# Kernel optimization log

Measured on AMD Instinct MI355X. Metric: run time of the kernel, lower is better.

## Reference

```python
import jax, jax.numpy as jnp
import numpy as np

N_S, N_T, E = 50000, 50000, 600000
D_IN, D_H, D_OUT = 256, 128, 64


def setup_inputs() -> dict:
    key = jax.random.key(0)
    k1, k2, k3, k4, k5, k6 = jax.random.split(key, 6)
    edge_src = jax.random.randint(k1, (E,), 0, N_S, dtype=jnp.int32)
    edge_dst = jax.random.randint(k2, (E,), 0, N_T, dtype=jnp.int32)
    edge_index = jnp.stack([edge_src, edge_dst], axis=0)  # [2, E]
    x_s = jax.random.normal(k3, (N_S, D_IN), dtype=jnp.float32)
    x_t = jax.random.normal(k4, (N_T, D_IN), dtype=jnp.float32)
    W0 = jax.random.normal(k5, (D_IN, D_H), dtype=jnp.float32) * (1.0 / np.sqrt(D_IN))
    W1 = jax.random.normal(k6, (D_H, D_OUT), dtype=jnp.float32) * (1.0 / np.sqrt(D_H))
    return {"edge_index": edge_index, "x_s": x_s, "x_t": x_t, "W0": W0, "W1": W1}


def gcn_conv(x, src, dst, W):
    """PyG GCNConv, bias=False: D^{-1/2}(A+I)D^{-1/2} (x @ W)."""
    N = x.shape[0]
    h = x @ W  # [N, out]
    loops = jnp.arange(N, dtype=src.dtype)
    s = jnp.concatenate([src, loops])  # add self-loops
    d = jnp.concatenate([dst, loops])
    deg = jax.ops.segment_sum(jnp.ones_like(d, dtype=h.dtype), d, num_segments=N)
    dinv = jnp.where(deg > 0, jax.lax.rsqrt(deg), 0.0)
    norm = dinv[s] * dinv[d]  # [E+N]
    return jax.ops.segment_sum(h[s] * norm[:, None], d, num_segments=N)


def reference(edge_index, x_s, x_t, W0, W1):
    n_s = x_s.shape[0]
    src = edge_index[0]
    dst = edge_index[1] + n_s  # targets live in the x_t block
    acts = [jax.nn.relu, lambda v: v]
    Ws = [W0, W1]
    for W, act in zip(Ws, acts):
        x = jnp.concatenate([x_s, x_t], axis=0)
        x = act(gcn_conv(x, src, dst, W))
        x_s, x_t = x[:n_s], x[n_s:]
    return (x_s, x_t)
```

## Files before the change

### kernel.cpp

```cpp
#include <hip/hip_runtime.h>
#include <cstdint>
#include <cstddef>

typedef unsigned short u16;
typedef unsigned int   u32;
typedef __attribute__((ext_vector_type(8))) short bf16x8;
typedef __attribute__((ext_vector_type(4))) float f32x4;

#define D_IN  256
#define D_H   128
#define D_OUT 64

__device__ __forceinline__ float bf2f(u16 u){
  union { u32 i; float f; } v; v.i = ((u32)u) << 16; return v.f;
}
__device__ __forceinline__ u16 f2bf(float f){
  union { float f; u32 i; } v; v.f = f;
  u32 r = (v.i + 0x7fffu + ((v.i >> 16) & 1u)) >> 16;
  return (u16)r;
}

__global__ void k_wprep(const float* __restrict__ W0, const float* __restrict__ W1,
                        u16* __restrict__ W0t, u16* __restrict__ W1t){
  int i = blockIdx.x * 256 + threadIdx.x;
  if (i < 128 * 256){
    int n = i >> 8, k = i & 255;
    W0t[i] = f2bf(W0[(size_t)k * 128 + n]);
  } else if (i < 128 * 256 + 64 * 128){
    int j = i - 128 * 256;
    int n = j >> 7, k = j & 127;
    W1t[j] = f2bf(W1[(size_t)k * 64 + n]);
  }
}

__global__ __launch_bounds__(256) void k_off(const int* __restrict__ deg, int N,
                                             int* __restrict__ off, int* __restrict__ cursor,
                                             float* __restrict__ dinv){
  __shared__ int s[256];
  __shared__ int sbase[256];
  const int tid = threadIdx.x;
  const int bid = blockIdx.x;
  const int i   = bid * 256 + tid;
  int acc = 0;
  const int lim = bid * 256;
  for (int j = tid; j < lim; j += 256) acc += deg[j];
  sbase[tid] = acc;
  int v = (i < N) ? deg[i] : 0;
  s[tid] = v;
  __syncthreads();
  for (int o = 128; o > 0; o >>= 1){
    if (tid < o) sbase[tid] += sbase[tid + o];
    __syncthreads();
  }
  for (int o = 1; o < 256; o <<= 1){
    int tv = (tid >= o) ? s[tid - o] : 0;
    __syncthreads();
    s[tid] += tv;
    __syncthreads();
  }
  if (i < N){
    int excl = s[tid] - v + sbase[0];
    off[i] = excl;
    cursor[i] = excl;
    dinv[i] = rsqrtf((float)v + 1.0f);
  }
}

__global__ void k_fill(const int* __restrict__ src, const int* __restrict__ dst,
                       int E, int* __restrict__ cursor, int* __restrict__ csr){
  int e = blockIdx.x * 256 + threadIdx.x;
  if (e < E){
    int d = dst[e];
    int p = atomicAdd(&cursor[d], 1);
    csr[p] = src[e];
  }
}

__global__ __launch_bounds__(512) void k_g1(
    const float* __restrict__ Xs, const float* __restrict__ Xt,
    const u16* __restrict__ W0t, int M, int n_s,
    const int* __restrict__ dst, int E, int* __restrict__ deg, int nbDeg,
    u16* __restrict__ out)
{
  __shared__ u16 Bs[128 * 256];
  const int t = threadIdx.x;

  if ((int)blockIdx.x < nbDeg){
    const int stride = nbDeg * 512;
    for (int e = blockIdx.x * 512 + t; e < E; e += stride)
      atomicAdd(&deg[dst[e]], 1);
    return;
  }

  const int wave = t >> 6, lane = t & 63;
  const int lm   = lane & 15, quad = lane >> 4;
  const int gw   = ((int)blockIdx.x - nbDeg) * 8 + wave;
  const int row  = gw * 16 + lm;

  int cr = (row < M) ? row : 0;
  const float* pa = ((cr < n_s) ? (Xs + (size_t)cr * D_IN)
                                : (Xt + (size_t)(cr - n_s) * D_IN)) + quad * 8;

  f32x4 A[16];
  asm volatile("global_load_dwordx4 %0, %1, off offset:0"   : "=v"(A[ 0]) : "v"(pa));
  asm volatile("global_load_dwordx4 %0, %1, off offset:16"  : "=v"(A[ 1]) : "v"(pa));
  asm volatile("global_load_dwordx4 %0, %1, off offset:128" : "=v"(A[ 2]) : "v"(pa));
  asm volatile("global_load_dwordx4 %0, %1, off offset:144" : "=v"(A[ 3]) : "v"(pa));
  asm volatile("global_load_dwordx4 %0, %1, off offset:256" : "=v"(A[ 4]) : "v"(pa));
  asm volatile("global_load_dwordx4 %0, %1, off offset:272" : "=v"(A[ 5]) : "v"(pa));
  asm volatile("global_load_dwordx4 %0, %1, off offset:384" : "=v"(A[ 6]) : "v"(pa));
  asm volatile("global_load_dwordx4 %0, %1, off offset:400" : "=v"(A[ 7]) : "v"(pa));
  asm volatile("global_load_dwordx4 %0, %1, off offset:512" : "=v"(A[ 8]) : "v"(pa));
  asm volatile("global_load_dwordx4 %0, %1, off offset:528" : "=v"(A[ 9]) : "v"(pa));
  asm volatile("global_load_dwordx4 %0, %1, off offset:640" : "=v"(A[10]) : "v"(pa));
  asm volatile("global_load_dwordx4 %0, %1, off offset:656" : "=v"(A[11]) : "v"(pa));
  asm volatile("global_load_dwordx4 %0, %1, off offset:768" : "=v"(A[12]) : "v"(pa));
  asm volatile("global_load_dwordx4 %0, %1, off offset:784" : "=v"(A[13]) : "v"(pa));
  asm volatile("global_load_dwordx4 %0, %1, off offset:896" : "=v"(A[14]) : "v"(pa));
  asm volatile("global_load_dwordx4 %0, %1, off offset:912" : "=v"(A[15]) : "v"(pa));

  {
    const int n = t >> 2;
    const int c = t & 3;
    const u16* wsrc = W0t + (size_t)n * 256 + c * 64;
    char* brow = (char*)Bs + n * 512;
    const int sw = (n & 15) << 4;
    #pragma unroll
    for (int j = 0; j < 8; j++){
      int off = (c * 128 + j * 16) ^ sw;
      *(int4*)(brow + off) = *(const int4*)(wsrc + j * 8);
    }
  }

  f32x4 acc[8];
  const f32x4 z = {0.f, 0.f, 0.f, 0.f};
  #pragma unroll
  for (int nf = 0; nf < 8; nf++) acc[nf] = z;

  __syncthreads();
  asm volatile("s_waitcnt vmcnt(0)" ::: "memory");
  __builtin_amdgcn_sched_barrier(0);

  const char* bb = (const char*)Bs + lm * 512;
  const int lmx = lm << 4;

  #pragma unroll
  for (int kk = 0; kk < 8; kk++){
    bf16x8 af;
    {
      f32x4 lo = A[2 * kk], hi = A[2 * kk + 1];
      u16 tmp[8];
      tmp[0] = f2bf(lo[0]); tmp[1] = f2bf(lo[1]);
      tmp[2] = f2bf(lo[2]); tmp[3] = f2bf(lo[3]);
      tmp[4] = f2bf(hi[0]); tmp[5] = f2bf(hi[1]);
      tmp[6] = f2bf(hi[2]); tmp[7] = f2bf(hi[3]);
      af = *(const bf16x8*)tmp;
    }
    const int koff = (kk * 64 + quad * 16) ^ lmx;
    #pragma unroll
    for (int nf = 0; nf < 8; nf++){
      bf16x8 bf = *(const bf16x8*)(bb + nf * 8192 + koff);
      acc[nf] = __builtin_amdgcn_mfma_f32_16x16x32_bf16(af, bf, acc[nf], 0, 0, 0);
    }
  }

  __syncthreads();
  u16* wreg = Bs + wave * 2048;
  #pragma unroll
  for (int nf = 0; nf < 8; nf++){
    #pragma unroll
    for (int rr = 0; rr < 4; rr++){
      int rl = quad * 4 + rr;
      int c  = nf * 16 + lm;
      wreg[rl * 128 + (c ^ (quad << 5))] = f2bf(acc[nf][rr]);
    }
  }
  {
    const int g = lane >> 4, l = lane & 15;
    const int wrow0 = gw * 16;
    #pragma unroll
    for (int i = 0; i < 4; i++){
      int rl = i * 4 + g;
      int m  = wrow0 + rl;
      bf16x8 v = *(const bf16x8*)&wreg[rl * 128 + ((l ^ (i << 2)) << 3)];
      if (m < M) *(bf16x8*)(out + (size_t)m * D_H + l * 8) = v;
    }
  }
}

__device__ __forceinline__ void aggf_body(
    const int* __restrict__ off, const int* __restrict__ deg,
    const int* __restrict__ csr, const float* __restrict__ dinv,
    u16* __restrict__ h1, int n_s, int n_t, int w, int lane)
{
  if (w >= n_t) return;
  const int g = lane >> 4;
  const int c = lane & 15;
  int start = off[w];
  int n     = deg[w];

  float r[8], p[8];
  #pragma unroll
  for (int q = 0; q < 8; q++){ r[q] = 0.f; p[q] = 0.f; }

  int i = 0;
  for (; i + 8 <= n; i += 8){
    int sa = csr[start + i + g];
    int sb = csr[start + i + 4 + g];
    int4 da = *(const int4*)(h1 + (size_t)sa * D_H + c * 8);
    int4 db = *(const int4*)(h1 + (size_t)sb * D_H + c * 8);
    const u16* ha = (const u16*)&da;
    const u16* hb = (const u16*)&db;
    #pragma unroll
    for (int q = 0; q < 8; q++){
      float va = bf2f(ha[q]), vb = bf2f(hb[q]);
      r[q] += va + vb;
      p[q] += fmaxf(va, 0.f) + fmaxf(vb, 0.f);
    }
  }
  for (; i < n; i += 4){
    if (i + g < n){
      int sa = csr[start + i + g];
      int4 da = *(const int4*)(h1 + (size_t)sa * D_H + c * 8);
      const u16* ha = (const u16*)&da;
      #pragma unroll
      for (int q = 0; q < 8; q++){
        float va = bf2f(ha[q]);
        r[q] += va;
        p[q] += fmaxf(va, 0.f);
      }
    }
  }

  #pragma unroll
  for (int q = 0; q < 8; q++){
    r[q] += __shfl_xor(r[q], 16, 64);
    r[q] += __shfl_xor(r[q], 32, 64);
    p[q] += __shfl_xor(p[q], 16, 64);
    p[q] += __shfl_xor(p[q], 32, 64);
  }

  if (g == 0){
    float di  = dinv[w];
    float di2 = di * di;
    u16* selfp = h1 + (size_t)(n_s + w) * D_H + c * 8;
    int4 hs = *(const int4*)selfp;
    const u16* hh = (const u16*)&hs;
    u16 ob[8];
    #pragma unroll
    for (int q = 0; q < 8; q++){
      float zq = fmaxf(di * r[q] + di2 * bf2f(hh[q]), 0.f);
      float uq = di * p[q] + di2 * zq;
      ob[q] = f2bf(uq);
    }
    *(int4*)selfp = *(int4*)ob;
  }
}

__device__ __forceinline__ bf16x8 relu_bf(int4 v, bool relu){
  const u16* s = (const u16*)&v;
  u16 tmp[8];
  #pragma unroll
  for (int q = 0; q < 8; q++){
    u16 x = s[q];
    tmp[q] = (relu && (x & 0x8000u)) ? (u16)0 : x;
  }
  return *(const bf16x8*)tmp;
}

__device__ __forceinline__ void gemm2_body(
    const u16* __restrict__ h1, const u16* __restrict__ W1t,
    int gb, int base, int rowLim, int n_s, float* __restrict__ out,
    u16* Bs, float* Cb)
{
  const int t    = threadIdx.x;
  const int wave = t >> 6, lane = t & 63;
  const int lm   = lane & 15, quad = lane >> 4;
  const int gw   = gb * 8 + wave;
  const int row  = base + gw * 16 + lm;

  int cr = (row < rowLim) ? row : base;
  const bool relu = (cr < n_s);
  const u16* pa = h1 + (size_t)cr * D_H + quad * 8;

  int4 a[4];
  a[0] = *(const int4*)(pa);
  a[1] = *(const int4*)(pa + 32);

  {
    const int n = t >> 3;
    const int c = t & 7;
    const u16* wsrc = W1t + (size_t)n * 128 + c * 16;
    char* brow = (char*)Bs + n * 256;
    const int sw = (n & 15) << 4;
    #pragma unroll
    for (int j = 0; j < 2; j++){
      int off = (c * 32 + j * 16) ^ sw;
      *(int4*)(brow + off) = *(const int4*)(wsrc + j * 8);
    }
  }
  a[2] = *(const int4*)(pa + 64);
  a[3] = *(const int4*)(pa + 96);
  __builtin_amdgcn_sched_barrier(0);

  f32x4 acc[4];
  const f32x4 z = {0.f, 0.f, 0.f, 0.f};
  #pragma unroll
  for (int nf = 0; nf < 4; nf++) acc[nf] = z;

  __syncthreads();

  const char* bb = (const char*)Bs + lm * 256;
  const int lmx = lm << 4;

  #pragma unroll
  for (int kk = 0; kk < 4; kk++){
    bf16x8 af = relu_bf(a[kk], relu);
    const int koff = (kk * 64 + quad * 16) ^ lmx;
    #pragma unroll
    for (int nf = 0; nf < 4; nf++){
      bf16x8 bf = *(const bf16x8*)(bb + nf * 4096 + koff);
      acc[nf] = __builtin_amdgcn_mfma_f32_16x16x32_bf16(af, bf, acc[nf], 0, 0, 0);
    }
  }

  float* wreg = Cb + wave * 1024;
  #pragma unroll
  for (int nf = 0; nf < 4; nf++){
    #pragma unroll
    for (int rr = 0; rr < 4; rr++){
      int rl = quad * 4 + rr;
      int c  = nf * 16 + lm;
      wreg[rl * 64 + (c ^ (quad << 4))] = acc[nf][rr];
    }
  }
  {
    const int g = lane >> 4, l = lane & 15;
    const int wrow0 = base + gw * 16;
    #pragma unroll
    for (int i = 0; i < 4; i++){
      int rl = i * 4 + g;
      int m  = wrow0 + rl;
      float4 v = *(const float4*)&wreg[rl * 64 + ((l ^ (i << 2)) << 2)];
      if (m < rowLim) *(float4*)(out + (size_t)m * D_OUT + l * 4) = v;
    }
  }
}

__global__ __launch_bounds__(512, 4) void k_agg2s(
    const int* __restrict__ off, const int* __restrict__ deg,
    const int* __restrict__ csr, const float* __restrict__ dinv,
    u16* __restrict__ h1, int n_s, int n_t,
    const u16* __restrict__ W1t, float* __restrict__ out, int nbAgg)
{
  __shared__ u16  Bs[64 * 128];
  __shared__ float Cb[8 * 1024];
  if ((int)blockIdx.x < nbAgg){
    int w = blockIdx.x * 8 + (threadIdx.x >> 6);
    aggf_body(off, deg, csr, dinv, h1, n_s, n_t, w, threadIdx.x & 63);
  } else {
    gemm2_body(h1, W1t, (int)blockIdx.x - nbAgg, 0, n_s, n_s, out, Bs, Cb);
  }
}

__global__ __launch_bounds__(512, 4) void k_g2t(
    const u16* __restrict__ h1, const u16* __restrict__ W1t,
    int M, int n_s, float* __restrict__ out)
{
  __shared__ u16  Bs[64 * 128];
  __shared__ float Cb[8 * 1024];
  gemm2_body(h1, W1t, (int)blockIdx.x, n_s, M, n_s, out, Bs, Cb);
}

static inline size_t alup(size_t x){ return (x + 255) & ~(size_t)255; }

extern "C" void kernel_launch(void* const* d_in, const int* in_sizes, int n_in,
                              void* d_out, int out_size, void* d_ws, size_t ws_size,
                              hipStream_t stream)
{
  const int*   ei = (const int*)d_in[0];
  const float* xs = (const float*)d_in[1];
  const float* xt = (const float*)d_in[2];
  const float* W0 = (const float*)d_in[3];
  const float* W1 = (const float*)d_in[4];
  const int E   = in_sizes[0] / 2;
  const int n_s = in_sizes[1] / D_IN;
  const int n_t = in_sizes[2] / D_IN;
  const int M   = n_s + n_t;
  const int* src = ei;
  const int* dst = ei + E;

  char* p = (char*)d_ws;
  int*   deg    = (int*)p;    p += alup((size_t)n_t * 4);
  int*   off    = (int*)p;    p += alup((size_t)n_t * 4);
  int*   cursor = (int*)p;    p += alup((size_t)n_t * 4);
  float* dinv   = (float*)p;  p += alup((size_t)n_t * 4);
  int*   csr    = (int*)p;    p += alup((size_t)E * 4);
  u16*   W0t    = (u16*)p;    p += alup((size_t)D_H * D_IN * 2);
  u16*   W1t    = (u16*)p;    p += alup((size_t)D_OUT * D_H * 2);
  u16*   h1     = (u16*)p;    p += alup((size_t)M * D_H * 2);

  const int nb_t   = (n_t + 255) / 256;
  const int nbDeg  = 128;
  const int nbG1   = (M + 127) / 128;
  const int nbAgg  = (n_t + 7) / 8;
  const int nbG2s  = (n_s + 127) / 128;
  const int nbG2t  = (n_t + 127) / 128;

  hipMemsetAsync(deg, 0, (size_t)n_t * 4, stream);
  k_wprep <<<160, 256, 0, stream>>>(W0, W1, W0t, W1t);
  k_g1    <<<nbDeg + nbG1, 512, 0, stream>>>(xs, xt, W0t, M, n_s, dst, E, deg, nbDeg, h1);
  k_off   <<<nb_t, 256, 0, stream>>>(deg, n_t, off, cursor, dinv);
  k_fill  <<<(E + 255) / 256, 256, 0, stream>>>(src, dst, E, cursor, csr);
  k_agg2s <<<nbAgg + nbG2s, 512, 0, stream>>>(off, deg, csr, dinv, h1, n_s, n_t,
                                              W1t, (float*)d_out, nbAgg);
  k_g2t   <<<nbG2t, 512, 0, stream>>>(h1, W1t, M, n_s, (float*)d_out);
}
```

Baseline: 267.4 us.

## Move degree count into weight-prep kernel and overlap CSR fill with GEMM1

The degree-counting atomics now share a launch with the weight transpose/convert kernel, and the CSR fill loop is folded into the first GEMM kernel as extra leading blocks, replacing the standalone fill kernel. The aim is to overlap the scattered-atomic CSR construction with the bandwidth-heavy feature GEMM and to drop one kernel launch. In exchange, the offset/scan kernel now sits between the prep and GEMM launches, so the degree pass no longer overlaps the GEMM, and the grid-stride fill with 128 blocks may serialize behind the GEMM blocks.

```diff
diff --git a/kernel.cpp b/kernel.cpp
--- a/kernel.cpp
+++ b/kernel.cpp
@@ -20,9 +20,19 @@
   return (u16)r;
 }
 
-__global__ void k_wprep(const float* __restrict__ W0, const float* __restrict__ W1,
-                        u16* __restrict__ W0t, u16* __restrict__ W1t){
-  int i = blockIdx.x * 256 + threadIdx.x;
+__global__ __launch_bounds__(512) void k_prep(
+    const float* __restrict__ W0, const float* __restrict__ W1,
+    u16* __restrict__ W0t, u16* __restrict__ W1t,
+    const int* __restrict__ dst, int E, int* __restrict__ deg, int nbDeg)
+{
+  const int t = threadIdx.x;
+  if ((int)blockIdx.x < nbDeg){
+    const int stride = nbDeg * 512;
+    for (int e = blockIdx.x * 512 + t; e < E; e += stride)
+      atomicAdd(&deg[dst[e]], 1);
+    return;
+  }
+  int i = ((int)blockIdx.x - nbDeg) * 512 + t;
   if (i < 128 * 256){
     int n = i >> 8, k = i & 255;
     W0t[i] = f2bf(W0[(size_t)k * 128 + n]);
@@ -66,35 +76,29 @@
   }
 }
 
-__global__ void k_fill(const int* __restrict__ src, const int* __restrict__ dst,
-                       int E, int* __restrict__ cursor, int* __restrict__ csr){
-  int e = blockIdx.x * 256 + threadIdx.x;
-  if (e < E){
-    int d = dst[e];
-    int p = atomicAdd(&cursor[d], 1);
-    csr[p] = src[e];
-  }
-}
-
-__global__ __launch_bounds__(512) void k_g1(
+__global__ __launch_bounds__(512) void k_g1f(
     const float* __restrict__ Xs, const float* __restrict__ Xt,
     const u16* __restrict__ W0t, int M, int n_s,
-    const int* __restrict__ dst, int E, int* __restrict__ deg, int nbDeg,
+    const int* __restrict__ src, const int* __restrict__ dst, int E,
+    int* __restrict__ cursor, int* __restrict__ csr, int nbFill,
     u16* __restrict__ out)
 {
   __shared__ u16 Bs[128 * 256];
   const int t = threadIdx.x;
 
-  if ((int)blockIdx.x < nbDeg){
-    const int stride = nbDeg * 512;
-    for (int e = blockIdx.x * 512 + t; e < E; e += stride)
-      atomicAdd(&deg[dst[e]], 1);
+  if ((int)blockIdx.x < nbFill){
+    const int stride = nbFill * 512;
+    for (int e = blockIdx.x * 512 + t; e < E; e += stride){
+      int d = dst[e];
+      int p = atomicAdd(&cursor[d], 1);
+      csr[p] = src[e];
+    }
     return;
   }
 
   const int wave = t >> 6, lane = t & 63;
   const int lm   = lane & 15, quad = lane >> 4;
-  const int gw   = ((int)blockIdx.x - nbDeg) * 8 + wave;
+  const int gw   = ((int)blockIdx.x - nbFill) * 8 + wave;
   const int row  = gw * 16 + lm;
 
   int cr = (row < M) ? row : 0;
@@ -402,16 +406,18 @@
 
   const int nb_t   = (n_t + 255) / 256;
   const int nbDeg  = 128;
+  const int nbW    = 80;
+  const int nbFill = 128;
   const int nbG1   = (M + 127) / 128;
   const int nbAgg  = (n_t + 7) / 8;
   const int nbG2s  = (n_s + 127) / 128;
   const int nbG2t  = (n_t + 127) / 128;
 
   hipMemsetAsync(deg, 0, (size_t)n_t * 4, stream);
-  k_wprep <<<160, 256, 0, stream>>>(W0, W1, W0t, W1t);
-  k_g1    <<<nbDeg + nbG1, 512, 0, stream>>>(xs, xt, W0t, M, n_s, dst, E, deg, nbDeg, h1);
+  k_prep  <<<nbDeg + nbW, 512, 0, stream>>>(W0, W1, W0t, W1t, dst, E, deg, nbDeg);
   k_off   <<<nb_t, 256, 0, stream>>>(deg, n_t, off, cursor, dinv);
-  k_fill  <<<(E + 255) / 256, 256, 0, stream>>>(src, dst, E, cursor, csr);
+  k_g1f   <<<nbFill + nbG1, 512, 0, stream>>>(xs, xt, W0t, M, n_s,
+                                              src, dst, E, cursor, csr, nbFill, h1);
   k_agg2s <<<nbAgg + nbG2s, 512, 0, stream>>>(off, deg, csr, dinv, h1, n_s, n_t,
                                               W1t, (float*)d_out, nbAgg);
   k_g2t   <<<nbG2t, 512, 0, stream>>>(h1, W1t, M, n_s, (float*)d_out);
```

After: 265.7 us. Within noise of the previous version (-0.6%).
